# Performance work log

Hardware: AMD Instinct MI355X
Metric: run time of the kernel (lower is better)

Reference implementation:

```python
import jax, jax.numpy as jnp
import numpy as np

T, N, E = 6, 50000, 1600000
NFEAT, NHID, NCLASS = 256, 256, 16
SLOPE = 11.0 / 48.0  # eval-mode RReLU: mean of default (lower=1/8, upper=1/3)


def _grcu(H_seq, src, dst, val, Wz, Uz, bz, Wr, Ur, br, Wh, Uh, bh, Q0):
    """One GRCU layer: matrix-GRU weight evolution + sparse GCN aggregation per step.
    H_seq: [T, N, in]  src/dst: [T, E] int  val: [T, E]  Q0: [in, out]."""
    n = H_seq.shape[1]

    def step(Q, xs):
        H, s, d, v = xs
        # mat_GRU_cell: x = hidden = prev_Q (z_topk path is unused in this repo's forward)
        z = jax.nn.sigmoid(Wz @ Q + Uz @ Q + bz)
        r = jax.nn.sigmoid(Wr @ Q + Ur @ Q + br)
        h = jnp.tanh(Wh @ Q + Uh @ (r * Q) + bh)
        Qn = (1.0 - z) * Q + z * h
        XW = H @ Qn                                   # [N, out]
        msg = v[:, None] * XW[s]                      # per-edge gather: Ahat row weights
        agg = jax.ops.segment_sum(msg, d, num_segments=n)  # Ahat @ (H @ Qn)
        out = jnp.where(agg >= 0, agg, SLOPE * agg)   # RReLU (eval)
        return Qn, out

    _, out_seq = jax.lax.scan(step, Q0, (H_seq, src, dst, val))
    return out_seq  # [T, N, out]


def setup_inputs() -> dict:
    key = jax.random.key(0)
    ks = iter(jax.random.split(key, 64))

    def rn(shape, scale=0.05):
        return jax.random.normal(next(ks), shape, dtype=jnp.float32) * scale

    inp = {
        "node_feats": jax.random.normal(next(ks), (T, N, NFEAT), dtype=jnp.float32),
        "edge_val": jax.random.uniform(next(ks), (T, E), dtype=jnp.float32),
    }
    for l, (fi, fo) in enumerate([(NFEAT, NHID), (NHID, NHID)]):
        for g in ("z", "r", "h"):
            inp[f"l{l}_W{g}"] = rn((fi, fi))
            inp[f"l{l}_U{g}"] = rn((fi, fi))
            inp[f"l{l}_b{g}"] = jnp.zeros((fi, fo), dtype=jnp.float32)
        inp[f"l{l}_Q0"] = rn((fi, fo))
    inp["mlp_W1"] = rn((NHID, NHID))
    inp["mlp_b1"] = jnp.zeros((NHID,), dtype=jnp.float32)
    inp["mlp_W2"] = rn((NHID, NCLASS))
    inp["mlp_b2"] = jnp.zeros((NCLASS,), dtype=jnp.float32)
    inp["edge_src"] = jax.random.randint(next(ks), (T, E), 0, N, dtype=jnp.int32)
    inp["edge_dst"] = jax.random.randint(next(ks), (T, E), 0, N, dtype=jnp.int32)
    return inp


def reference(node_feats, edge_val,
              l0_Wz, l0_Uz, l0_bz, l0_Wr, l0_Ur, l0_br, l0_Wh, l0_Uh, l0_bh, l0_Q0,
              l1_Wz, l1_Uz, l1_bz, l1_Wr, l1_Ur, l1_br, l1_Wh, l1_Uh, l1_bh, l1_Q0,
              mlp_W1, mlp_b1, mlp_W2, mlp_b2,
              edge_src, edge_dst):
    h1 = _grcu(node_feats, edge_src, edge_dst, edge_val,
               l0_Wz, l0_Uz, l0_bz, l0_Wr, l0_Ur, l0_br, l0_Wh, l0_Uh, l0_bh, l0_Q0)
    h2 = _grcu(h1, edge_src, edge_dst, edge_val,
               l1_Wz, l1_Uz, l1_bz, l1_Wr, l1_Ur, l1_br, l1_Wh, l1_Uh, l1_bh, l1_Q0)
    out = h2[-1]                                    # last timestep, [N, nhid]
    hid = jax.nn.relu(out @ mlp_W1 + mlp_b1)
    logits = hid @ mlp_W2 + mlp_b2
    return jax.nn.log_softmax(logits, axis=1)       # [N, nclass]
```

## Files before the change

kernel.cpp:

```cpp
#include <hip/hip_runtime.h>
#include <cstddef>

#define SLOPE_F (11.0f / 48.0f)

static const int NN = 50000;
static const int EE = 1600000;
static const int D  = 256;
static const int NCH = 196;
static const int GB  = 391;

typedef __attribute__((ext_vector_type(8))) short short8;
typedef __attribute__((ext_vector_type(4))) float f32x4;

__device__ __forceinline__ ushort f2bf(float f) {
    unsigned u = __float_as_uint(f);
    unsigned r = (u + 0x7fffu + ((u >> 16) & 1u)) >> 16;
    return (ushort)r;
}
__device__ __forceinline__ float bf2f(ushort u) {
    return __uint_as_float(((unsigned)u) << 16);
}

__global__ __launch_bounds__(256) void prephist_kernel(
        const float* __restrict__ Wz0, const float* __restrict__ Uz0,
        const float* __restrict__ Wr0, const float* __restrict__ Ur0,
        const float* __restrict__ Wh0, const float* __restrict__ Uh0,
        const float* __restrict__ Wz1, const float* __restrict__ Uz1,
        const float* __restrict__ Wr1, const float* __restrict__ Ur1,
        const float* __restrict__ Wh1, const float* __restrict__ Uh1,
        const float* __restrict__ W1,
        ushort* __restrict__ WB, ushort* __restrict__ BtW1,
        const int* __restrict__ dst, int* __restrict__ deg) {
    int b = blockIdx.x;
    int tid = threadIdx.x;
    if (b >= 144) {
        int e = (b - 144) * 256 + tid;
        if (e < EE) atomicAdd(&deg[dst[e]], 1);
        return;
    }
    __shared__ float lt[64][65];
    if (b < 128) {
        int mat = b >> 4;
        int tr = (b >> 2) & 3, tc = b & 3;
        const float* P = nullptr; const float* S = nullptr;
        switch (mat) {
            case 0: P = Wz0; S = Uz0; break;
            case 1: P = Wr0; S = Ur0; break;
            case 2: P = Wh0; break;
            case 3: P = Uh0; break;
            case 4: P = Wz1; S = Uz1; break;
            case 5: P = Wr1; S = Ur1; break;
            case 6: P = Wh1; break;
            default: P = Uh1; break;
        }
#pragma unroll
        for (int r0 = 0; r0 < 64; r0 += 4) {
            int r = r0 + (tid >> 6);
            int c = tid & 63;
            int row = tr * 64 + r, col = tc * 64 + c;
            float v = P[row * 256 + col];
            if (S) v += S[row * 256 + col];
            lt[r][c] = v;
        }
        __syncthreads();
#pragma unroll
        for (int c0 = 0; c0 < 64; c0 += 4) {
            int c = c0 + (tid >> 6);
            int r = tid & 63;
            WB[(size_t)mat * 65536 + (size_t)(tc * 64 + c) * 256 + tr * 64 + r] =
                f2bf(lt[r][c]);
        }
    } else {
        int t = b - 128;
        int tr = (t >> 2) & 3, tc = t & 3;
#pragma unroll
        for (int r0 = 0; r0 < 64; r0 += 4) {
            int r = r0 + (tid >> 6);
            int c = tid & 63;
            lt[r][c] = W1[(tr * 64 + r) * 256 + tc * 64 + c];
        }
        __syncthreads();
#pragma unroll
        for (int c0 = 0; c0 < 64; c0 += 4) {
            int c = c0 + (tid >> 6);
            int r = tid & 63;
            BtW1[(size_t)(tc * 64 + c) * 256 + tr * 64 + r] = f2bf(lt[r][c]);
        }
    }
}

__global__ __launch_bounds__(256) void gruscan_kernel(
        const ushort* __restrict__ WB,
        const float* __restrict__ bz0, const float* __restrict__ br0,
        const float* __restrict__ bh0, const float* __restrict__ Q00,
        const float* __restrict__ bz1, const float* __restrict__ br1,
        const float* __restrict__ bh1, const float* __restrict__ Q01,
        ushort* __restrict__ Bt,
        const int* __restrict__ deg, int* __restrict__ rs, int* __restrict__ cur,
        int* __restrict__ bsum, int* __restrict__ boff, int* __restrict__ done) {
    int tid = threadIdx.x;
    if (blockIdx.x >= 512) {
        __shared__ int wsum[4];
        __shared__ int lastflag;
        int blk = blockIdx.x - 512;
        int i = blk * 256 + tid;
        int lane = tid & 63, wv = tid >> 6;
        int v = (i < NN) ? deg[i] : 0;
        int x = v;
#pragma unroll
        for (int off = 1; off < 64; off <<= 1) {
            int t = __shfl_up(x, off, 64);
            if (lane >= off) x += t;
        }
        if (lane == 63) wsum[wv] = x;
        __syncthreads();
        if (tid == 0) {
            int s = 0;
#pragma unroll
            for (int q = 0; q < 4; ++q) { int t = wsum[q]; wsum[q] = s; s += t; }
            bsum[blk] = s;
        }
        __syncthreads();
        if (i < NN) { int p = wsum[wv] + x - v; rs[i] = p; cur[i] = p; }
        __threadfence();
        if (tid == 0) lastflag = (atomicAdd(done, 1) == NCH - 1);
        __syncthreads();
        if (lastflag) {
            __threadfence();
            int bv = (tid < NCH) ? bsum[tid] : 0;
            int bx = bv;
#pragma unroll
            for (int off = 1; off < 64; off <<= 1) {
                int t = __shfl_up(bx, off, 64);
                if (lane >= off) bx += t;
            }
            if (lane == 63) wsum[wv] = bx;
            __syncthreads();
            if (tid == 0) {
                int s = 0;
#pragma unroll
                for (int q = 0; q < 4; ++q) { int t = wsum[q]; wsum[q] = s; s += t; }
            }
            __syncthreads();
            if (tid < NCH) boff[tid] = wsum[wv] + bx - bv;
        }
        return;
    }
    __shared__ float qs[256];
    __shared__ float rqs[256];
    int layer = blockIdx.x >> 8;
    int j = blockIdx.x & 255;
    int i = tid;
    const ushort* Mz = WB + ((size_t)layer * 4 + 0) * 65536;
    const ushort* Mr = WB + ((size_t)layer * 4 + 1) * 65536;
    const ushort* Wh = WB + ((size_t)layer * 4 + 2) * 65536;
    const ushort* Uh = WB + ((size_t)layer * 4 + 3) * 65536;
    const float* bz = layer ? bz1 : bz0;
    const float* br = layer ? br1 : br0;
    const float* bh = layer ? bh1 : bh0;
    const float* Q0 = layer ? Q01 : Q00;

    float bzv = bz[i * 256 + j];
    float brv = br[i * 256 + j];
    float bhv = bh[i * 256 + j];

    qs[i] = Q0[i * 256 + j];
    __syncthreads();

    for (int step = 0; step < 6; ++step) {
        float az = 0.f, ar = 0.f, ah = 0.f;
#pragma unroll 8
        for (int k = 0; k < 256; ++k) {
            float q = qs[k];
            az += bf2f(Mz[k * 256 + i]) * q;
            ar += bf2f(Mr[k * 256 + i]) * q;
            ah += bf2f(Wh[k * 256 + i]) * q;
        }
        float zz = 1.f / (1.f + expf(-(az + bzv)));
        float rr = 1.f / (1.f + expf(-(ar + brv)));
        float qo = qs[i];
        rqs[i] = rr * qo;
        __syncthreads();
        float bu = 0.f;
#pragma unroll 8
        for (int k = 0; k < 256; ++k)
            bu += bf2f(Uh[k * 256 + i]) * rqs[k];
        float h = tanhf(ah + bu + bhv);
        float qn = (1.f - zz) * qo + zz * h;
        qs[i] = qn;
        __syncthreads();
    }
    Bt[(size_t)layer * 65536 + (size_t)j * 256 + i] = f2bf(qs[i]);
}

template <int ASRC, int EPI>
__device__ __forceinline__ void gemm_body(int bid, int tid,
                                          const ushort* __restrict__ A,
                                          const float* __restrict__ Af,
                                          const ushort* __restrict__ Bt,
                                          const float* __restrict__ bias,
                                          ushort* __restrict__ C, int M) {
    int w = tid >> 6, l = tid & 63;
    int lr = l & 15;
    int lk = l >> 4;
    int row0 = bid * 128 + w * 32;
    int ra = row0 + lr;      if (ra > M - 1) ra = M - 1;
    int rb = row0 + 16 + lr; if (rb > M - 1) rb = M - 1;
    const ushort* Ap0  = A  + (size_t)ra * 256 + lk * 8;
    const ushort* Ap1  = A  + (size_t)rb * 256 + lk * 8;
    const float*  Apf0 = Af + (size_t)ra * 256 + lk * 8;
    const float*  Apf1 = Af + (size_t)rb * 256 + lk * 8;
    const ushort* Bp   = Bt + (size_t)lr * 256 + lk * 8;

    f32x4 acc0[16] = {};
    f32x4 acc1[16] = {};
#pragma unroll
    for (int kc = 0; kc < 8; ++kc) {
        short8 a0, a1;
        if (ASRC == 0) {
            a0 = *(const short8*)(Ap0 + kc * 32);
            a1 = *(const short8*)(Ap1 + kc * 32);
        } else {
            float4 f0 = *(const float4*)(Apf0 + kc * 32);
            float4 f1 = *(const float4*)(Apf0 + kc * 32 + 4);
            float4 g0 = *(const float4*)(Apf1 + kc * 32);
            float4 g1 = *(const float4*)(Apf1 + kc * 32 + 4);
            a0[0] = (short)f2bf(f0.x); a0[1] = (short)f2bf(f0.y);
            a0[2] = (short)f2bf(f0.z); a0[3] = (short)f2bf(f0.w);
            a0[4] = (short)f2bf(f1.x); a0[5] = (short)f2bf(f1.y);
            a0[6] = (short)f2bf(f1.z); a0[7] = (short)f2bf(f1.w);
            a1[0] = (short)f2bf(g0.x); a1[1] = (short)f2bf(g0.y);
            a1[2] = (short)f2bf(g0.z); a1[3] = (short)f2bf(g0.w);
            a1[4] = (short)f2bf(g1.x); a1[5] = (short)f2bf(g1.y);
            a1[6] = (short)f2bf(g1.z); a1[7] = (short)f2bf(g1.w);
        }
#pragma unroll
        for (int nb = 0; nb < 16; ++nb) {
            short8 bf = *(const short8*)(Bp + (size_t)nb * 4096 + kc * 32);
            acc0[nb] = __builtin_amdgcn_mfma_f32_16x16x32_bf16(a0, bf, acc0[nb], 0, 0, 0);
            acc1[nb] = __builtin_amdgcn_mfma_f32_16x16x32_bf16(a1, bf, acc1[nb], 0, 0, 0);
        }
    }

    int ro = lk * 4;
#pragma unroll
    for (int nb = 0; nb < 16; ++nb) {
        int gc = nb * 16 + lr;
        float bb = (EPI == 1) ? bias[gc] : 0.f;
#pragma unroll
        for (int q = 0; q < 4; ++q) {
            int g0 = row0 + ro + q;
            if (g0 < M) {
                float v = acc0[nb][q];
                if (EPI == 1) v = fmaxf(v + bb, 0.f);
                C[(size_t)g0 * 256 + gc] = f2bf(v);
            }
            int g1 = row0 + 16 + ro + q;
            if (g1 < M) {
                float v = acc1[nb][q];
                if (EPI == 1) v = fmaxf(v + bb, 0.f);
                C[(size_t)g1 * 256 + gc] = f2bf(v);
            }
        }
    }
}

template <int ASRC, int EPI>
__global__ __launch_bounds__(256) void gemm_mfma(const ushort* __restrict__ A,
                                                 const float* __restrict__ Af,
                                                 const ushort* __restrict__ Bt,
                                                 const float* __restrict__ bias,
                                                 ushort* __restrict__ C, int M) {
    gemm_body<ASRC, EPI>(blockIdx.x, threadIdx.x, A, Af, Bt, bias, C, M);
}

__global__ __launch_bounds__(256) void gemsca_kernel(const float* __restrict__ Af,
                                                     const ushort* __restrict__ Bt,
                                                     ushort* __restrict__ C, int M,
                                                     const int* __restrict__ src,
                                                     const int* __restrict__ dst,
                                                     const float* __restrict__ val,
                                                     int* __restrict__ cur,
                                                     const int* __restrict__ boff,
                                                     unsigned long long* __restrict__ csr) {
    if (blockIdx.x < GB) {
        gemm_body<1, 0>(blockIdx.x, threadIdx.x, nullptr, Af, Bt, nullptr, C, M);
        return;
    }
    int e = (blockIdx.x - GB) * 256 + threadIdx.x;
    if (e < EE) {
        int d = dst[e];
        int p = atomicAdd(&cur[d], 1) + boff[d >> 8];
        unsigned long long pk = (unsigned long long)(unsigned)src[e]
                              | ((unsigned long long)(unsigned)__float_as_uint(val[e]) << 32);
        __builtin_nontemporal_store(pk, &csr[p]);
    }
}

__global__ __launch_bounds__(256) void agg_csr_kernel(const ushort* __restrict__ XW,
                                                      const int2* __restrict__ csr,
                                                      const int* __restrict__ rs,
                                                      const int* __restrict__ boff,
                                                      ushort* __restrict__ out) {
    int d = blockIdx.x * 4 + (threadIdx.x >> 6);
    if (d >= NN) return;
    int l = threadIdx.x & 63;
    int h = l >> 5;
    int il = l & 31;
    int beg = rs[d] + boff[d >> 8];
    int end = (d + 1 < NN) ? (rs[d + 1] + boff[(d + 1) >> 8]) : EE;
    float a0 = 0.f, a1 = 0.f, a2 = 0.f, a3 = 0.f;
    float a4 = 0.f, a5 = 0.f, a6 = 0.f, a7 = 0.f;
    int i = beg + h;
    for (; i + 14 < end; i += 16) {
        int2 e[8];
        short8 x[8];
#pragma unroll
        for (int u = 0; u < 8; ++u) e[u] = csr[i + 2 * u];
#pragma unroll
        for (int u = 0; u < 8; ++u)
            x[u] = *(const short8*)&XW[(size_t)e[u].x * D + il * 8];
#pragma unroll
        for (int u = 0; u < 8; ++u) {
            float v = __int_as_float(e[u].y);
            a0 += v * bf2f((ushort)x[u][0]);
            a1 += v * bf2f((ushort)x[u][1]);
            a2 += v * bf2f((ushort)x[u][2]);
            a3 += v * bf2f((ushort)x[u][3]);
            a4 += v * bf2f((ushort)x[u][4]);
            a5 += v * bf2f((ushort)x[u][5]);
            a6 += v * bf2f((ushort)x[u][6]);
            a7 += v * bf2f((ushort)x[u][7]);
        }
    }
    for (; i + 6 < end; i += 8) {
        int2 e[4];
        short8 x[4];
#pragma unroll
        for (int u = 0; u < 4; ++u) e[u] = csr[i + 2 * u];
#pragma unroll
        for (int u = 0; u < 4; ++u)
            x[u] = *(const short8*)&XW[(size_t)e[u].x * D + il * 8];
#pragma unroll
        for (int u = 0; u < 4; ++u) {
            float v = __int_as_float(e[u].y);
            a0 += v * bf2f((ushort)x[u][0]);
            a1 += v * bf2f((ushort)x[u][1]);
            a2 += v * bf2f((ushort)x[u][2]);
            a3 += v * bf2f((ushort)x[u][3]);
            a4 += v * bf2f((ushort)x[u][4]);
            a5 += v * bf2f((ushort)x[u][5]);
            a6 += v * bf2f((ushort)x[u][6]);
            a7 += v * bf2f((ushort)x[u][7]);
        }
    }
    for (; i < end; i += 2) {
        int2 e0 = csr[i];
        float v0 = __int_as_float(e0.y);
        short8 x0 = *(const short8*)&XW[(size_t)e0.x * D + il * 8];
        a0 += v0 * bf2f((ushort)x0[0]); a1 += v0 * bf2f((ushort)x0[1]);
        a2 += v0 * bf2f((ushort)x0[2]); a3 += v0 * bf2f((ushort)x0[3]);
        a4 += v0 * bf2f((ushort)x0[4]); a5 += v0 * bf2f((ushort)x0[5]);
        a6 += v0 * bf2f((ushort)x0[6]); a7 += v0 * bf2f((ushort)x0[7]);
    }
    a0 += __shfl_xor(a0, 32); a1 += __shfl_xor(a1, 32);
    a2 += __shfl_xor(a2, 32); a3 += __shfl_xor(a3, 32);
    a4 += __shfl_xor(a4, 32); a5 += __shfl_xor(a5, 32);
    a6 += __shfl_xor(a6, 32); a7 += __shfl_xor(a7, 32);
    if (h == 0) {
        float r[8] = {a0, a1, a2, a3, a4, a5, a6, a7};
        short8 o;
#pragma unroll
        for (int c = 0; c < 8; ++c) {
            float v = r[c];
            v = (v >= 0.f) ? v : SLOPE_F * v;
            o[c] = (short)f2bf(v);
        }
        *(short8*)&out[(size_t)d * D + il * 8] = o;
    }
}

__global__ void mlp2_kernel(const ushort* __restrict__ hid, const float* __restrict__ W2,
                            const float* __restrict__ b2, float* __restrict__ out, int M) {
    int tid = threadIdx.x;
    int n = blockIdx.x * 16 + (tid >> 4);
    int c = tid & 15;
    if (n >= M) return;
    float acc = b2[c];
    const ushort* hp = hid + (size_t)n * D;
    for (int k = 0; k < D; k += 8) {
        short8 h8 = *(const short8*)(hp + k);
#pragma unroll
        for (int u = 0; u < 8; ++u)
            acc += bf2f((ushort)h8[u]) * W2[(k + u) * 16 + c];
    }
    float m = acc;
#pragma unroll
    for (int off = 1; off < 16; off <<= 1)
        m = fmaxf(m, __shfl_xor(m, off, 16));
    float ex = expf(acc - m);
    float s = ex;
#pragma unroll
    for (int off = 1; off < 16; off <<= 1)
        s += __shfl_xor(s, off, 16);
    out[(size_t)n * 16 + c] = acc - m - logf(s);
}

extern "C" void kernel_launch(void* const* d_in, const int* in_sizes, int n_in,
                              void* d_out, int out_size, void* d_ws, size_t ws_size,
                              hipStream_t stream) {
    const float* node_feats = (const float*)d_in[0];
    const float* edge_val   = (const float*)d_in[1];
    const float* l0_Wz = (const float*)d_in[2];
    const float* l0_Uz = (const float*)d_in[3];
    const float* l0_bz = (const float*)d_in[4];
    const float* l0_Wr = (const float*)d_in[5];
    const float* l0_Ur = (const float*)d_in[6];
    const float* l0_br = (const float*)d_in[7];
    const float* l0_Wh = (const float*)d_in[8];
    const float* l0_Uh = (const float*)d_in[9];
    const float* l0_bh = (const float*)d_in[10];
    const float* l0_Q0 = (const float*)d_in[11];
    const float* l1_Wz = (const float*)d_in[12];
    const float* l1_Uz = (const float*)d_in[13];
    const float* l1_bz = (const float*)d_in[14];
    const float* l1_Wr = (const float*)d_in[15];
    const float* l1_Ur = (const float*)d_in[16];
    const float* l1_br = (const float*)d_in[17];
    const float* l1_Wh = (const float*)d_in[18];
    const float* l1_Uh = (const float*)d_in[19];
    const float* l1_bh = (const float*)d_in[20];
    const float* l1_Q0 = (const float*)d_in[21];
    const float* W1 = (const float*)d_in[22];
    const float* b1 = (const float*)d_in[23];
    const float* W2 = (const float*)d_in[24];
    const float* b2 = (const float*)d_in[25];
    const int* e_src = (const int*)d_in[26];
    const int* e_dst = (const int*)d_in[27];
    float* out = (float*)d_out;

    const size_t BIG = (size_t)NN * D;
    ushort* XWb = (ushort*)d_ws;
    ushort* H   = XWb + BIG;
    ushort* Bt  = H + BIG;
    ushort* WB  = Bt + 3 * 65536;
    int2*   csr = (int2*)(WB + 8 * 65536);
    int*    deg = (int*)(csr + EE);
    int*    done = deg + NN;
    int*    rs  = done + 1;
    int*    cur = rs + NN;
    int*    bsum = cur + NN;
    int*    boff = bsum + 200;

    const float* feats5 = node_feats + (size_t)5 * BIG;
    const int*   src5   = e_src + (size_t)5 * EE;
    const int*   dst5   = e_dst + (size_t)5 * EE;
    const float* val5   = edge_val + (size_t)5 * EE;

    hipMemsetAsync(deg, 0, (NN + 1) * sizeof(int), stream);

    const int histblocks = (EE + 255) / 256;
    prephist_kernel<<<144 + histblocks, 256, 0, stream>>>(
        l0_Wz, l0_Uz, l0_Wr, l0_Ur, l0_Wh, l0_Uh,
        l1_Wz, l1_Uz, l1_Wr, l1_Ur, l1_Wh, l1_Uh,
        W1, WB, Bt + 2 * 65536, dst5, deg);

    gruscan_kernel<<<512 + NCH, 256, 0, stream>>>(WB, l0_bz, l0_br, l0_bh, l0_Q0,
                                                  l1_bz, l1_br, l1_bh, l1_Q0, Bt,
                                                  deg, rs, cur, bsum, boff, done);

    gemsca_kernel<<<GB + histblocks, 256, 0, stream>>>(feats5, Bt + 0 * 65536, XWb, NN,
                                                       src5, dst5, val5, cur, boff,
                                                       (unsigned long long*)csr);

    const int ablocks = (NN + 3) / 4;

    agg_csr_kernel<<<ablocks, 256, 0, stream>>>(XWb, csr, rs, boff, H);

    gemm_mfma<0, 0><<<GB, 256, 0, stream>>>(H, nullptr, Bt + 1 * 65536, nullptr, XWb, NN);
    agg_csr_kernel<<<ablocks, 256, 0, stream>>>(XWb, csr, rs, boff, H);

    gemm_mfma<0, 1><<<GB, 256, 0, stream>>>(H, nullptr, Bt + 2 * 65536, b1, XWb, NN);
    mlp2_kernel<<<(NN + 15) / 16, 256, 0, stream>>>(XWb, W2, b2, out, NN);
}
```

Baseline: 682.9 us.

## Fuse CSR aggregation with following GEMM and MLP head via LDS tiles

Replaces the separate aggregation, GEMM, and MLP2 kernels with a fused kernel. Each 64-row block aggregates its rows into a swizzled LDS tile, then runs the MFMA GEMM against the next layer's weights straight from LDS. For the final layer it also applies the bias/ReLU, the 16-class projection, and log-softmax in place. This removes the round trips of the intermediate H/hidden matrices through global memory and cuts kernel launches. In exchange, each row is now aggregated by a half-wave with no split across edges, and the 32KB of LDS per block may reduce occupancy for the gather-bound phase. A redundant __syncthreads is also added in the GRU scan.

```diff
diff --git a/kernel.cpp b/kernel.cpp
--- a/kernel.cpp
+++ b/kernel.cpp
@@ -8,6 +8,7 @@
 static const int D  = 256;
 static const int NCH = 196;
 static const int GB  = 391;
+static const int AB  = 782;
 
 typedef __attribute__((ext_vector_type(8))) short short8;
 typedef __attribute__((ext_vector_type(4))) float f32x4;
@@ -187,27 +188,23 @@
             bu += bf2f(Uh[k * 256 + i]) * rqs[k];
         float h = tanhf(ah + bu + bhv);
         float qn = (1.f - zz) * qo + zz * h;
+        __syncthreads();
         qs[i] = qn;
         __syncthreads();
     }
     Bt[(size_t)layer * 65536 + (size_t)j * 256 + i] = f2bf(qs[i]);
 }
 
-template <int ASRC, int EPI>
-__device__ __forceinline__ void gemm_body(int bid, int tid,
-                                          const ushort* __restrict__ A,
-                                          const float* __restrict__ Af,
-                                          const ushort* __restrict__ Bt,
-                                          const float* __restrict__ bias,
-                                          ushort* __restrict__ C, int M) {
+__device__ __forceinline__ void gemm0_body(int bid, int tid,
+                                           const float* __restrict__ Af,
+                                           const ushort* __restrict__ Bt,
+                                           ushort* __restrict__ C, int M) {
     int w = tid >> 6, l = tid & 63;
     int lr = l & 15;
     int lk = l >> 4;
     int row0 = bid * 128 + w * 32;
     int ra = row0 + lr;      if (ra > M - 1) ra = M - 1;
     int rb = row0 + 16 + lr; if (rb > M - 1) rb = M - 1;
-    const ushort* Ap0  = A  + (size_t)ra * 256 + lk * 8;
-    const ushort* Ap1  = A  + (size_t)rb * 256 + lk * 8;
     const float*  Apf0 = Af + (size_t)ra * 256 + lk * 8;
     const float*  Apf1 = Af + (size_t)rb * 256 + lk * 8;
     const ushort* Bp   = Bt + (size_t)lr * 256 + lk * 8;
@@ -217,23 +214,18 @@
 #pragma unroll
     for (int kc = 0; kc < 8; ++kc) {
         short8 a0, a1;
-        if (ASRC == 0) {
-            a0 = *(const short8*)(Ap0 + kc * 32);
-            a1 = *(const short8*)(Ap1 + kc * 32);
-        } else {
-            float4 f0 = *(const float4*)(Apf0 + kc * 32);
-            float4 f1 = *(const float4*)(Apf0 + kc * 32 + 4);
-            float4 g0 = *(const float4*)(Apf1 + kc * 32);
-            float4 g1 = *(const float4*)(Apf1 + kc * 32 + 4);
-            a0[0] = (short)f2bf(f0.x); a0[1] = (short)f2bf(f0.y);
-            a0[2] = (short)f2bf(f0.z); a0[3] = (short)f2bf(f0.w);
-            a0[4] = (short)f2bf(f1.x); a0[5] = (short)f2bf(f1.y);
-            a0[6] = (short)f2bf(f1.z); a0[7] = (short)f2bf(f1.w);
-            a1[0] = (short)f2bf(g0.x); a1[1] = (short)f2bf(g0.y);
-            a1[2] = (short)f2bf(g0.z); a1[3] = (short)f2bf(g0.w);
-            a1[4] = (short)f2bf(g1.x); a1[5] = (short)f2bf(g1.y);
-            a1[6] = (short)f2bf(g1.z); a1[7] = (short)f2bf(g1.w);
-        }
+        float4 f0 = *(const float4*)(Apf0 + kc * 32);
+        float4 f1 = *(const float4*)(Apf0 + kc * 32 + 4);
+        float4 g0 = *(const float4*)(Apf1 + kc * 32);
+        float4 g1 = *(const float4*)(Apf1 + kc * 32 + 4);
+        a0[0] = (short)f2bf(f0.x); a0[1] = (short)f2bf(f0.y);
+        a0[2] = (short)f2bf(f0.z); a0[3] = (short)f2bf(f0.w);
+        a0[4] = (short)f2bf(f1.x); a0[5] = (short)f2bf(f1.y);
+        a0[6] = (short)f2bf(f1.z); a0[7] = (short)f2bf(f1.w);
+        a1[0] = (short)f2bf(g0.x); a1[1] = (short)f2bf(g0.y);
+        a1[2] = (short)f2bf(g0.z); a1[3] = (short)f2bf(g0.w);
+        a1[4] = (short)f2bf(g1.x); a1[5] = (short)f2bf(g1.y);
+        a1[6] = (short)f2bf(g1.z); a1[7] = (short)f2bf(g1.w);
 #pragma unroll
         for (int nb = 0; nb < 16; ++nb) {
             short8 bf = *(const short8*)(Bp + (size_t)nb * 4096 + kc * 32);
@@ -246,32 +238,14 @@
 #pragma unroll
     for (int nb = 0; nb < 16; ++nb) {
         int gc = nb * 16 + lr;
-        float bb = (EPI == 1) ? bias[gc] : 0.f;
 #pragma unroll
         for (int q = 0; q < 4; ++q) {
             int g0 = row0 + ro + q;
-            if (g0 < M) {
-                float v = acc0[nb][q];
-                if (EPI == 1) v = fmaxf(v + bb, 0.f);
-                C[(size_t)g0 * 256 + gc] = f2bf(v);
-            }
+            if (g0 < M) C[(size_t)g0 * 256 + gc] = f2bf(acc0[nb][q]);
             int g1 = row0 + 16 + ro + q;
-            if (g1 < M) {
-                float v = acc1[nb][q];
-                if (EPI == 1) v = fmaxf(v + bb, 0.f);
-                C[(size_t)g1 * 256 + gc] = f2bf(v);
-            }
-        }
-    }
-}
-
-template <int ASRC, int EPI>
-__global__ __launch_bounds__(256) void gemm_mfma(const ushort* __restrict__ A,
-                                                 const float* __restrict__ Af,
-                                                 const ushort* __restrict__ Bt,
-                                                 const float* __restrict__ bias,
-                                                 ushort* __restrict__ C, int M) {
-    gemm_body<ASRC, EPI>(blockIdx.x, threadIdx.x, A, Af, Bt, bias, C, M);
+            if (g1 < M) C[(size_t)g1 * 256 + gc] = f2bf(acc1[nb][q]);
+        }
+    }
 }
 
 __global__ __launch_bounds__(256) void gemsca_kernel(const float* __restrict__ Af,
@@ -284,7 +258,7 @@
                                                      const int* __restrict__ boff,
                                                      unsigned long long* __restrict__ csr) {
     if (blockIdx.x < GB) {
-        gemm_body<1, 0>(blockIdx.x, threadIdx.x, nullptr, Af, Bt, nullptr, C, M);
+        gemm0_body(blockIdx.x, threadIdx.x, Af, Bt, C, M);
         return;
     }
     int e = (blockIdx.x - GB) * 256 + threadIdx.x;
@@ -297,113 +271,145 @@
     }
 }
 
-__global__ __launch_bounds__(256) void agg_csr_kernel(const ushort* __restrict__ XW,
-                                                      const int2* __restrict__ csr,
-                                                      const int* __restrict__ rs,
-                                                      const int* __restrict__ boff,
-                                                      ushort* __restrict__ out) {
-    int d = blockIdx.x * 4 + (threadIdx.x >> 6);
-    if (d >= NN) return;
-    int l = threadIdx.x & 63;
-    int h = l >> 5;
-    int il = l & 31;
-    int beg = rs[d] + boff[d >> 8];
-    int end = (d + 1 < NN) ? (rs[d + 1] + boff[(d + 1) >> 8]) : EE;
-    float a0 = 0.f, a1 = 0.f, a2 = 0.f, a3 = 0.f;
-    float a4 = 0.f, a5 = 0.f, a6 = 0.f, a7 = 0.f;
-    int i = beg + h;
-    for (; i + 14 < end; i += 16) {
-        int2 e[8];
-        short8 x[8];
-#pragma unroll
-        for (int u = 0; u < 8; ++u) e[u] = csr[i + 2 * u];
-#pragma unroll
-        for (int u = 0; u < 8; ++u)
-            x[u] = *(const short8*)&XW[(size_t)e[u].x * D + il * 8];
-#pragma unroll
-        for (int u = 0; u < 8; ++u) {
-            float v = __int_as_float(e[u].y);
-            a0 += v * bf2f((ushort)x[u][0]);
-            a1 += v * bf2f((ushort)x[u][1]);
-            a2 += v * bf2f((ushort)x[u][2]);
-            a3 += v * bf2f((ushort)x[u][3]);
-            a4 += v * bf2f((ushort)x[u][4]);
-            a5 += v * bf2f((ushort)x[u][5]);
-            a6 += v * bf2f((ushort)x[u][6]);
-            a7 += v * bf2f((ushort)x[u][7]);
-        }
-    }
-    for (; i + 6 < end; i += 8) {
-        int2 e[4];
-        short8 x[4];
-#pragma unroll
-        for (int u = 0; u < 4; ++u) e[u] = csr[i + 2 * u];
-#pragma unroll
-        for (int u = 0; u < 4; ++u)
-            x[u] = *(const short8*)&XW[(size_t)e[u].x * D + il * 8];
-#pragma unroll
-        for (int u = 0; u < 4; ++u) {
-            float v = __int_as_float(e[u].y);
-            a0 += v * bf2f((ushort)x[u][0]);
-            a1 += v * bf2f((ushort)x[u][1]);
-            a2 += v * bf2f((ushort)x[u][2]);
-            a3 += v * bf2f((ushort)x[u][3]);
-            a4 += v * bf2f((ushort)x[u][4]);
-            a5 += v * bf2f((ushort)x[u][5]);
-            a6 += v * bf2f((ushort)x[u][6]);
-            a7 += v * bf2f((ushort)x[u][7]);
-        }
-    }
-    for (; i < end; i += 2) {
-        int2 e0 = csr[i];
-        float v0 = __int_as_float(e0.y);
-        short8 x0 = *(const short8*)&XW[(size_t)e0.x * D + il * 8];
-        a0 += v0 * bf2f((ushort)x0[0]); a1 += v0 * bf2f((ushort)x0[1]);
-        a2 += v0 * bf2f((ushort)x0[2]); a3 += v0 * bf2f((ushort)x0[3]);
-        a4 += v0 * bf2f((ushort)x0[4]); a5 += v0 * bf2f((ushort)x0[5]);
-        a6 += v0 * bf2f((ushort)x0[6]); a7 += v0 * bf2f((ushort)x0[7]);
-    }
-    a0 += __shfl_xor(a0, 32); a1 += __shfl_xor(a1, 32);
-    a2 += __shfl_xor(a2, 32); a3 += __shfl_xor(a3, 32);
-    a4 += __shfl_xor(a4, 32); a5 += __shfl_xor(a5, 32);
-    a6 += __shfl_xor(a6, 32); a7 += __shfl_xor(a7, 32);
-    if (h == 0) {
-        float r[8] = {a0, a1, a2, a3, a4, a5, a6, a7};
-        short8 o;
-#pragma unroll
-        for (int c = 0; c < 8; ++c) {
-            float v = r[c];
-            v = (v >= 0.f) ? v : SLOPE_F * v;
-            o[c] = (short)f2bf(v);
-        }
-        *(short8*)&out[(size_t)d * D + il * 8] = o;
-    }
-}
-
-__global__ void mlp2_kernel(const ushort* __restrict__ hid, const float* __restrict__ W2,
-                            const float* __restrict__ b2, float* __restrict__ out, int M) {
+template <int EPI>
+__global__ __launch_bounds__(256) void aggemm_kernel(
+        const ushort* __restrict__ XW,
+        const int2* __restrict__ csr,
+        const int* __restrict__ rs, const int* __restrict__ boff,
+        const ushort* __restrict__ Bt, const float* __restrict__ bias,
+        const float* __restrict__ W2, const float* __restrict__ b2,
+        ushort* __restrict__ C, float* __restrict__ out) {
+    __shared__ ushort Hl[64 * 256];
     int tid = threadIdx.x;
-    int n = blockIdx.x * 16 + (tid >> 4);
-    int c = tid & 15;
-    if (n >= M) return;
-    float acc = b2[c];
-    const ushort* hp = hid + (size_t)n * D;
-    for (int k = 0; k < D; k += 8) {
-        short8 h8 = *(const short8*)(hp + k);
-#pragma unroll
-        for (int u = 0; u < 8; ++u)
-            acc += bf2f((ushort)h8[u]) * W2[(k + u) * 16 + c];
-    }
-    float m = acc;
-#pragma unroll
-    for (int off = 1; off < 16; off <<= 1)
-        m = fmaxf(m, __shfl_xor(m, off, 16));
-    float ex = expf(acc - m);
-    float s = ex;
-#pragma unroll
-    for (int off = 1; off < 16; off <<= 1)
-        s += __shfl_xor(s, off, 16);
-    out[(size_t)n * 16 + c] = acc - m - logf(s);
+    int row0 = blockIdx.x * 64;
+
+    int hw = tid >> 5;
+    int il = tid & 31;
+#pragma unroll
+    for (int q = 0; q < 8; ++q) {
+        int d = row0 + hw * 8 + q;
+        int lrow = hw * 8 + q;
+        char* dstp = (char*)Hl + lrow * 512 + ((il * 16) ^ ((lrow & 7) << 4));
+        if (d < NN) {
+            int beg = rs[d] + boff[d >> 8];
+            int end = (d + 1 < NN) ? (rs[d + 1] + boff[(d + 1) >> 8]) : EE;
+            float a0 = 0.f, a1 = 0.f, a2 = 0.f, a3 = 0.f;
+            float a4 = 0.f, a5 = 0.f, a6 = 0.f, a7 = 0.f;
+            int i = beg;
+            for (; i + 7 < end; i += 8) {
+                int2 e[8];
+                short8 x[8];
+#pragma unroll
+                for (int u = 0; u < 8; ++u) e[u] = csr[i + u];
+#pragma unroll
+                for (int u = 0; u < 8; ++u)
+                    x[u] = *(const short8*)&XW[(size_t)e[u].x * D + il * 8];
+#pragma unroll
+                for (int u = 0; u < 8; ++u) {
+                    float v = __int_as_float(e[u].y);
+                    a0 += v * bf2f((ushort)x[u][0]);
+                    a1 += v * bf2f((ushort)x[u][1]);
+                    a2 += v * bf2f((ushort)x[u][2]);
+                    a3 += v * bf2f((ushort)x[u][3]);
+                    a4 += v * bf2f((ushort)x[u][4]);
+                    a5 += v * bf2f((ushort)x[u][5]);
+                    a6 += v * bf2f((ushort)x[u][6]);
+                    a7 += v * bf2f((ushort)x[u][7]);
+                }
+            }
+            for (; i < end; ++i) {
+                int2 e0 = csr[i];
+                float v = __int_as_float(e0.y);
+                short8 x0 = *(const short8*)&XW[(size_t)e0.x * D + il * 8];
+                a0 += v * bf2f((ushort)x0[0]); a1 += v * bf2f((ushort)x0[1]);
+                a2 += v * bf2f((ushort)x0[2]); a3 += v * bf2f((ushort)x0[3]);
+                a4 += v * bf2f((ushort)x0[4]); a5 += v * bf2f((ushort)x0[5]);
+                a6 += v * bf2f((ushort)x0[6]); a7 += v * bf2f((ushort)x0[7]);
+            }
+            float r[8] = {a0, a1, a2, a3, a4, a5, a6, a7};
+            short8 o;
+#pragma unroll
+            for (int c = 0; c < 8; ++c) {
+                float v = r[c];
+                v = (v >= 0.f) ? v : SLOPE_F * v;
+                o[c] = (short)f2bf(v);
+            }
+            *(short8*)dstp = o;
+        } else {
+            short8 z = {};
+            *(short8*)dstp = z;
+        }
+    }
+    __syncthreads();
+
+    int w = tid >> 6, l = tid & 63;
+    int lr = l & 15, lk = l >> 4;
+    int arow = w * 16 + lr;
+    const char* Ab = (const char*)Hl + arow * 512;
+    int asw = (arow & 7) << 4;
+    const ushort* Bp = Bt + (size_t)lr * 256 + lk * 8;
+
+    f32x4 acc[16] = {};
+#pragma unroll
+    for (int kc = 0; kc < 8; ++kc) {
+        short8 a = *(const short8*)(Ab + ((kc * 64 + lk * 16) ^ asw));
+#pragma unroll
+        for (int nb = 0; nb < 16; ++nb) {
+            short8 bf = *(const short8*)(Bp + (size_t)nb * 4096 + kc * 32);
+            acc[nb] = __builtin_amdgcn_mfma_f32_16x16x32_bf16(a, bf, acc[nb], 0, 0, 0);
+        }
+    }
+
+    int ro = lk * 4;
+    if (EPI == 0) {
+#pragma unroll
+        for (int nb = 0; nb < 16; ++nb) {
+            int gc = nb * 16 + lr;
+#pragma unroll
+            for (int q = 0; q < 4; ++q) {
+                int g = row0 + w * 16 + ro + q;
+                if (g < NN) C[(size_t)g * 256 + gc] = f2bf(acc[nb][q]);
+            }
+        }
+    } else {
+#pragma unroll
+        for (int nb = 0; nb < 16; ++nb) {
+            int gc = nb * 16 + lr;
+            float bb = bias[gc];
+#pragma unroll
+            for (int q = 0; q < 4; ++q) {
+                int lrow = w * 16 + ro + q;
+                float v = fmaxf(acc[nb][q] + bb, 0.f);
+                *(ushort*)((char*)Hl + lrow * 512 + ((gc * 2) ^ ((lrow & 7) << 4))) = f2bf(v);
+            }
+        }
+        __syncthreads();
+        float b2v = b2[tid & 15];
+#pragma unroll
+        for (int it = 0; it < 4; ++it) {
+            int r = it * 16 + (tid >> 4);
+            int c = tid & 15;
+            int g = row0 + r;
+            int sw2 = (r & 7) << 4;
+            float acc2 = b2v;
+            for (int k8 = 0; k8 < 32; ++k8) {
+                short8 hv = *(const short8*)((const char*)Hl + r * 512 + ((k8 * 16) ^ sw2));
+#pragma unroll
+                for (int u = 0; u < 8; ++u)
+                    acc2 += bf2f((ushort)hv[u]) * W2[(k8 * 8 + u) * 16 + c];
+            }
+            float m = acc2;
+#pragma unroll
+            for (int off = 1; off < 16; off <<= 1)
+                m = fmaxf(m, __shfl_xor(m, off, 16));
+            float ex = expf(acc2 - m);
+            float s = ex;
+#pragma unroll
+            for (int off = 1; off < 16; off <<= 1)
+                s += __shfl_xor(s, off, 16);
+            if (g < NN) out[(size_t)g * 16 + c] = acc2 - m - logf(s);
+        }
+    }
 }
 
 extern "C" void kernel_launch(void* const* d_in, const int* in_sizes, int n_in,
@@ -473,13 +479,9 @@
                                                        src5, dst5, val5, cur, boff,
                                                        (unsigned long long*)csr);
 
-    const int ablocks = (NN + 3) / 4;
-
-    agg_csr_kernel<<<ablocks, 256, 0, stream>>>(XWb, csr, rs, boff, H);
-
-    gemm_mfma<0, 0><<<GB, 256, 0, stream>>>(H, nullptr, Bt + 1 * 65536, nullptr, XWb, NN);
-    agg_csr_kernel<<<ablocks, 256, 0, stream>>>(XWb, csr, rs, boff, H);
-
-    gemm_mfma<0, 1><<<GB, 256, 0, stream>>>(H, nullptr, Bt + 2 * 65536, b1, XWb, NN);
-    mlp2_kernel<<<(NN + 15) / 16, 256, 0, stream>>>(XWb, W2, b2, out, NN);
-}
+    aggemm_kernel<0><<<AB, 256, 0, stream>>>(XWb, csr, rs, boff, Bt + 1 * 65536,
+                                             nullptr, nullptr, nullptr, H, nullptr);
+
+    aggemm_kernel<1><<<AB, 256, 0, stream>>>(H, csr, rs, boff, Bt + 2 * 65536,
+                                             b1, W2, b2, nullptr, out);
+}
```

Measured after the change: 774.8 us. 13.5% more time.
